# Kernel tuning notes

Hardware: AMD Instinct MI355X
Metric: run time of the kernel (lower is better)

## Reference

```python
import jax, jax.numpy as jnp
import numpy as np

# Contact model constants (from ContactModel defaults / hardcoded values)
STIFFNESS = 100000.0
DISSIPATION = 0.2
STATIC_FRICTION = 0.8
DYNAMIC_FRICTION = 0.8
VISCOUS_FRICTION = 0.5
TRANSITION_VELOCITY = 0.2
GROUND_HEIGHT = 0.0
DT = 0.05
RADIUS = 0.032
EPS = 1e-5
EPS2 = 1e-16
BV = 50.0
BD = 300.0

# 12 spheres: 6 right (bodies 4,5), 6 left (bodies 9,10)
SPHERE_BODY = np.array([4, 4, 4, 4, 5, 5, 9, 9, 9, 9, 10, 10], dtype=np.int32)
SPHERE_LOCAL = np.array([
    [0.00190115788407966, -0.01, -0.00382630379623308],
    [0.148386399942063,   -0.01, -0.028713422052654],
    [0.133001170607051,   -0.01,  0.0516362473449566],
    [0.0662346661991635,  -0.01,  0.0263641606741698],
    [0.06,                -0.01, -0.0187603084619177],
    [0.045,               -0.01,  0.0618569567549652],
    [0.00190115788407966, -0.01,  0.00382630379623308],
    [0.148386399942063,   -0.01,  0.028713422052654],
    [0.133001170607051,   -0.01, -0.0516362473449566],
    [0.0662346661991635,  -0.01, -0.0263641606741698],
    [0.06,                -0.01,  0.0187603084619177],
    [0.045,               -0.01, -0.0618569567549652],
], dtype=np.float32)
NORMAL = np.array([0.0, 1.0, 0.0], dtype=np.float32)


def _sphere_positions(joints, joints_ori):
    # joints: (B,24,3), joints_ori: (B,24,3,3) -> (B,12,3)
    body_pos = joints[:, SPHERE_BODY]            # (B,12,3)
    body_ori = joints_ori[:, SPHERE_BODY]        # (B,12,3,3)
    local = jnp.asarray(SPHERE_LOCAL)
    return body_pos + jnp.einsum('bsij,sj->bsi', body_ori, local)


def _contact_forces(pos, vel):
    # pos, vel: (B,S,3) -> forces (B,S,3); fully vectorized over spheres
    n = jnp.asarray(NORMAL)
    indentation = GROUND_HEIGHT - pos[..., 1]                    # (B,S)
    vnormal = vel[..., 1]                                        # dot(vel, [0,1,0])
    vtangent = vel - vnormal[..., None] * n                      # (B,S,3)
    ind_vel = -vnormal
    k = 0.5 * STIFFNESS ** (2.0 / 3.0)
    # sqrt(ind^2+eps)**1.5 == (ind^2+eps)**0.75
    fH = (4.0 / 3.0) * k * np.sqrt(RADIUS * k) * (indentation * indentation + EPS) ** 0.75
    fHd = fH * (1.0 + 1.5 * DISSIPATION * ind_vel)
    fn = ((0.5 * jnp.tanh(BV * (ind_vel + 1.0 / (1.5 * DISSIPATION))) + 0.5 + EPS2)
          * (0.5 * jnp.tanh(BD * indentation) + 0.5 + EPS2) * fHd)
    vslip = jnp.sqrt(jnp.sum(vtangent * vtangent, axis=-1) + EPS)
    vrel = vslip / TRANSITION_VELOCITY
    ffriction = fn * (jnp.minimum(vrel, 1.0)
                      * (DYNAMIC_FRICTION + 2.0 * (STATIC_FRICTION - DYNAMIC_FRICTION) / (1.0 + vrel * vrel))
                      + VISCOUS_FRICTION * vslip)
    force = fn[..., None] * n
    friction_force = ffriction[..., None] * (-vtangent) / (vslip[..., None] + EPS)
    return force + friction_force


def _cop_and_torque(pos, forces):
    # pos, forces: (B,S,3) -> cop (B,3), torque (B,3); vectorized batch version of the per-b loop
    vf = forces[..., 1]                          # (B,S)
    valid = vf > 0.0
    w = jnp.where(valid, vf, 0.0)
    tw = jnp.sum(w, axis=-1)                     # (B,)
    has = tw > 0.0
    tw_safe = jnp.where(has, tw, 1.0)
    cop_x = jnp.where(has, jnp.sum(pos[..., 0] * w, axis=-1) / tw_safe, 0.0)
    cop_y = jnp.where(has, GROUND_HEIGHT, 0.0)
    cop_z = jnp.where(has, jnp.sum(pos[..., 2] * w, axis=-1) / tw_safe, 0.0)
    cop = jnp.stack([cop_x, cop_y, cop_z], axis=-1)  # (B,3)
    r = pos - cop[:, None, :]
    f_masked = jnp.where(valid[..., None], forces, 0.0)  # only valid contacts contribute torque
    torque = jnp.sum(jnp.cross(r, f_masked), axis=1)
    return cop, torque


def setup_inputs() -> dict:
    key = jax.random.key(0)
    k1, k2 = jax.random.split(key)
    B = 262144
    joints = jax.random.normal(k1, (B, 24, 3), dtype=jnp.float32)
    joints_ori = jax.random.normal(k2, (B, 24, 3, 3), dtype=jnp.float32)
    return {"joints": joints, "joints_ori": joints_ori}


def reference(joints, joints_ori):
    pos = _sphere_positions(joints, joints_ori)              # (B,12,3)
    # finite-difference sphere velocity over frames (dt); zero at first frame
    vel = (pos - jnp.concatenate([pos[:1], pos[:-1]], axis=0)) / DT
    sphere_forces = _contact_forces(pos, vel)                # (B,12,3)

    force = jnp.sum(sphere_forces, axis=1)
    force_right = jnp.sum(sphere_forces[:, :6], axis=1)
    force_left = jnp.sum(sphere_forces[:, 6:], axis=1)
    cop, torque = _cop_and_torque(pos, sphere_forces)
    cop_right, torque_right = _cop_and_torque(pos[:, :6], sphere_forces[:, :6])
    cop_left, torque_left = _cop_and_torque(pos[:, 6:], sphere_forces[:, 6:])
    return (force, torque, cop, sphere_forces, pos,
            force_right, force_left, torque_right, torque_left, cop_right, cop_left)
```

## Files before the change

kernel.cpp:

```cpp
#include <hip/hip_runtime.h>
#include <math.h>


__device__ __constant__ float c_local[12][3] = {
    {0.00190115788407966f, -0.01f, -0.00382630379623308f},
    {0.148386399942063f,   -0.01f, -0.028713422052654f},
    {0.133001170607051f,   -0.01f,  0.0516362473449566f},
    {0.0662346661991635f,  -0.01f,  0.0263641606741698f},
    {0.06f,                -0.01f, -0.0187603084619177f},
    {0.045f,               -0.01f,  0.0618569567549652f},
    {0.00190115788407966f, -0.01f,  0.00382630379623308f},
    {0.148386399942063f,   -0.01f,  0.028713422052654f},
    {0.133001170607051f,   -0.01f, -0.0516362473449566f},
    {0.0662346661991635f,  -0.01f, -0.0263641606741698f},
    {0.06f,                -0.01f,  0.0187603084619177f},
    {0.045f,               -0.01f, -0.0618569567549652f}};

__global__ __launch_bounds__(256)
void contact_kernel(const float* __restrict__ joints,
                    const float* __restrict__ jori,
                    float* __restrict__ out, const int B)
{
    const int b = blockIdx.x * blockDim.x + threadIdx.x;
    if (b >= B) return;

    float px[12], py[12], pz[12];
    float fx[12], fy[12], fz[12];

    {
        const int bodies[4] = {4, 5, 9, 10};
        const int sbeg[4]   = {0, 4, 6, 10};
        const int scnt[4]   = {4, 2, 4, 2};
        const int bp = (b > 0) ? (b - 1) : b;
        const float* jr  = joints + (size_t)b  * 72;
        const float* jrp = joints + (size_t)bp * 72;
        const float* mr  = jori   + (size_t)b  * 216;
        const float* mrp = jori   + (size_t)bp * 216;

        #pragma unroll
        for (int bi = 0; bi < 4; ++bi) {
            const int body = bodies[bi];
            const float jx = jr[body*3+0], jy = jr[body*3+1], jz = jr[body*3+2];
            const float* m = mr + body*9;
            const float m00=m[0],m01=m[1],m02=m[2];
            const float m10=m[3],m11=m[4],m12=m[5];
            const float m20=m[6],m21=m[7],m22=m[8];
            const float kx = jrp[body*3+0], ky = jrp[body*3+1], kz = jrp[body*3+2];
            const float* nn = mrp + body*9;
            const float n00=nn[0],n01=nn[1],n02=nn[2];
            const float n10=nn[3],n11=nn[4],n12=nn[5];
            const float n20=nn[6],n21=nn[7],n22=nn[8];
            #pragma unroll
            for (int si = 0; si < 4; ++si) {
                if (si < scnt[bi]) {
                    const int s = sbeg[bi] + si;
                    const float lx = c_local[s][0];
                    const float ly = c_local[s][1];
                    const float lz = c_local[s][2];
                    const float ax = jx + m00*lx + m01*ly + m02*lz;
                    const float ay = jy + m10*lx + m11*ly + m12*lz;
                    const float az = jz + m20*lx + m21*ly + m22*lz;
                    const float bx = kx + n00*lx + n01*ly + n02*lz;
                    const float by = ky + n10*lx + n11*ly + n12*lz;
                    const float bz = kz + n20*lx + n21*ly + n22*lz;
                    px[s] = ax; py[s] = ay; pz[s] = az;
                    fx[s] = (ax - bx) * 20.0f;
                    fy[s] = (ay - by) * 20.0f;
                    fz[s] = (az - bz) * 20.0f;
                }
            }
        }
    }

    const float KF  = 1077.21734501594f;
    const float CFH = (4.0f/3.0f) * KF * sqrtf(0.032f * KF);
    #pragma unroll
    for (int s = 0; s < 12; ++s) {
        const float vx = fx[s], vy = fy[s], vz = fz[s];
        const float ind     = -py[s];
        const float ind_vel = -vy;
        const float q   = ind*ind + 1e-5f;
        const float fH  = CFH * sqrtf(q * sqrtf(q));
        const float fHd = fH * (1.0f + 0.3f * ind_vel);
        const float t1 = (0.5f*tanhf(50.0f*(ind_vel + 3.3333333333333335f)) + 0.5f) + 1e-16f;
        const float t2 = (0.5f*tanhf(300.0f*ind) + 0.5f) + 1e-16f;
        const float fn = t1 * t2 * fHd;
        const float vslip = sqrtf(vx*vx + vz*vz + 1e-5f);
        const float vrel  = vslip * 5.0f;
        const float mu  = fminf(vrel, 1.0f) * 0.8f + 0.5f * vslip;
        const float ffr = fn * mu;
        const float sc  = ffr / (vslip + 1e-5f);
        fx[s] = -sc * vx;
        fy[s] = fn;
        fz[s] = -sc * vz;
    }

    float res[3][9];
    const int gs0[3] = {0, 0, 6};
    const int gs1[3] = {12, 6, 12};
    #pragma unroll
    for (int g = 0; g < 3; ++g) {
        float Fx=0.f, Fy=0.f, Fz=0.f, tw=0.f, sx=0.f, sz=0.f;
        #pragma unroll
        for (int s = 0; s < 12; ++s) {
            if (s >= gs0[g] && s < gs1[g]) {
                Fx += fx[s]; Fy += fy[s]; Fz += fz[s];
                const float w = fy[s] > 0.f ? fy[s] : 0.f;
                tw += w;
                sx += px[s] * w;
                sz += pz[s] * w;
            }
        }
        const bool has = tw > 0.f;
        const float cx = has ? sx / tw : 0.f;
        const float cz = has ? sz / tw : 0.f;
        float Tx=0.f, Ty=0.f, Tz=0.f;
        #pragma unroll
        for (int s = 0; s < 12; ++s) {
            if (s >= gs0[g] && s < gs1[g]) {
                if (fy[s] > 0.f) {
                    const float rx = px[s]-cx, ry = py[s], rz = pz[s]-cz;
                    Tx += ry*fz[s] - rz*fy[s];
                    Ty += rz*fx[s] - rx*fz[s];
                    Tz += rx*fy[s] - ry*fx[s];
                }
            }
        }
        res[g][0]=Fx; res[g][1]=Fy; res[g][2]=Fz;
        res[g][3]=Tx; res[g][4]=Ty; res[g][5]=Tz;
        res[g][6]=cx; res[g][7]=0.f; res[g][8]=cz;
    }

    const size_t sB = (size_t)B;
    const size_t t3 = (size_t)b * 3;
    float* o;
    o = out;           o[t3]=res[0][0]; o[t3+1]=res[0][1]; o[t3+2]=res[0][2];
    o = out + sB*3;    o[t3]=res[0][3]; o[t3+1]=res[0][4]; o[t3+2]=res[0][5];
    o = out + sB*6;    o[t3]=res[0][6]; o[t3+1]=res[0][7]; o[t3+2]=res[0][8];
    o = out + sB*81;   o[t3]=res[1][0]; o[t3+1]=res[1][1]; o[t3+2]=res[1][2];
    o = out + sB*84;   o[t3]=res[2][0]; o[t3+1]=res[2][1]; o[t3+2]=res[2][2];
    o = out + sB*87;   o[t3]=res[1][3]; o[t3+1]=res[1][4]; o[t3+2]=res[1][5];
    o = out + sB*90;   o[t3]=res[2][3]; o[t3+1]=res[2][4]; o[t3+2]=res[2][5];
    o = out + sB*93;   o[t3]=res[1][6]; o[t3+1]=res[1][7]; o[t3+2]=res[1][8];
    o = out + sB*96;   o[t3]=res[2][6]; o[t3+1]=res[2][7]; o[t3+2]=res[2][8];

    float* osf = out + sB*9  + (size_t)b*36;
    float* opp = out + sB*45 + (size_t)b*36;
    if ((B & 3) == 0) {
        float bufF[36], bufP[36];
        #pragma unroll
        for (int s = 0; s < 12; ++s) {
            bufF[s*3+0]=fx[s]; bufF[s*3+1]=fy[s]; bufF[s*3+2]=fz[s];
            bufP[s*3+0]=px[s]; bufP[s*3+1]=py[s]; bufP[s*3+2]=pz[s];
        }
        #pragma unroll
        for (int i = 0; i < 9; ++i) {
            reinterpret_cast<float4*>(osf)[i] = reinterpret_cast<float4*>(bufF)[i];
            reinterpret_cast<float4*>(opp)[i] = reinterpret_cast<float4*>(bufP)[i];
        }
    } else {
        #pragma unroll
        for (int s = 0; s < 12; ++s) {
            osf[s*3+0]=fx[s]; osf[s*3+1]=fy[s]; osf[s*3+2]=fz[s];
            opp[s*3+0]=px[s]; opp[s*3+1]=py[s]; opp[s*3+2]=pz[s];
        }
    }
}

extern "C" void kernel_launch(void* const* d_in, const int* in_sizes, int n_in,
                              void* d_out, int out_size, void* d_ws, size_t ws_size,
                              hipStream_t stream) {
    const float* joints = (const float*)d_in[0];
    const float* jori   = (const float*)d_in[1];
    float* out = (float*)d_out;
    const int B = in_sizes[0] / 72;
    const int block = 256;
    const int grid  = (B + block - 1) / block;
    contact_kernel<<<grid, block, 0, stream>>>(joints, jori, out, B);
}
```

Baseline: 67.31 us.

## Reuse previous-frame sphere positions via wavefront shuffle instead of reloading

Each 64-lane wavefront now covers 63 consecutive frames plus one halo lane. The previous frame's sphere positions come from __shfl_up across lanes, so the second set of joint and orientation loads and the duplicate transform math are gone. Halo lanes compute but do not write, and frame 0 gets zero velocity because shuffling from lane 0 returns its own value. The constant-memory offset table is replaced by in-register constants. The cost is about 1/64 redundant compute and a new launch-geometry mapping.

```diff
diff --git a/kernel.cpp b/kernel.cpp
--- a/kernel.cpp
+++ b/kernel.cpp
@@ -1,42 +1,36 @@
 #include <hip/hip_runtime.h>
 #include <math.h>
 
-
-__device__ __constant__ float c_local[12][3] = {
-    {0.00190115788407966f, -0.01f, -0.00382630379623308f},
-    {0.148386399942063f,   -0.01f, -0.028713422052654f},
-    {0.133001170607051f,   -0.01f,  0.0516362473449566f},
-    {0.0662346661991635f,  -0.01f,  0.0263641606741698f},
-    {0.06f,                -0.01f, -0.0187603084619177f},
-    {0.045f,               -0.01f,  0.0618569567549652f},
-    {0.00190115788407966f, -0.01f,  0.00382630379623308f},
-    {0.148386399942063f,   -0.01f,  0.028713422052654f},
-    {0.133001170607051f,   -0.01f, -0.0516362473449566f},
-    {0.0662346661991635f,  -0.01f, -0.0263641606741698f},
-    {0.06f,                -0.01f,  0.0187603084619177f},
-    {0.045f,               -0.01f, -0.0618569567549652f}};
 
 __global__ __launch_bounds__(256)
 void contact_kernel(const float* __restrict__ joints,
                     const float* __restrict__ jori,
                     float* __restrict__ out, const int B)
 {
-    const int b = blockIdx.x * blockDim.x + threadIdx.x;
-    if (b >= B) return;
+    const int lane = threadIdx.x & 63;
+    const int wg   = blockIdx.x * 4 + (threadIdx.x >> 6);
+    const long bL  = (long)wg * 63 + lane;
+    const bool do_write = (bL < B) && (lane > 0 || bL == 0);
+    const int  b = (bL < (long)B) ? (int)bL : (B - 1);
 
     float px[12], py[12], pz[12];
     float fx[12], fy[12], fz[12];
 
     {
+        const float c_lx[12] = {0.00190115788407966f, 0.148386399942063f, 0.133001170607051f,
+                                0.0662346661991635f, 0.06f, 0.045f,
+                                0.00190115788407966f, 0.148386399942063f, 0.133001170607051f,
+                                0.0662346661991635f, 0.06f, 0.045f};
+        const float c_lz[12] = {-0.00382630379623308f, -0.028713422052654f, 0.0516362473449566f,
+                                 0.0263641606741698f, -0.0187603084619177f, 0.0618569567549652f,
+                                 0.00382630379623308f, 0.028713422052654f, -0.0516362473449566f,
+                                -0.0263641606741698f, 0.0187603084619177f, -0.0618569567549652f};
+        const float ly = -0.01f;
         const int bodies[4] = {4, 5, 9, 10};
         const int sbeg[4]   = {0, 4, 6, 10};
         const int scnt[4]   = {4, 2, 4, 2};
-        const int bp = (b > 0) ? (b - 1) : b;
-        const float* jr  = joints + (size_t)b  * 72;
-        const float* jrp = joints + (size_t)bp * 72;
-        const float* mr  = jori   + (size_t)b  * 216;
-        const float* mrp = jori   + (size_t)bp * 216;
-
+        const float* jr = joints + (size_t)b * 72;
+        const float* mr = jori   + (size_t)b * 216;
         #pragma unroll
         for (int bi = 0; bi < 4; ++bi) {
             const int body = bodies[bi];
@@ -45,31 +39,24 @@
             const float m00=m[0],m01=m[1],m02=m[2];
             const float m10=m[3],m11=m[4],m12=m[5];
             const float m20=m[6],m21=m[7],m22=m[8];
-            const float kx = jrp[body*3+0], ky = jrp[body*3+1], kz = jrp[body*3+2];
-            const float* nn = mrp + body*9;
-            const float n00=nn[0],n01=nn[1],n02=nn[2];
-            const float n10=nn[3],n11=nn[4],n12=nn[5];
-            const float n20=nn[6],n21=nn[7],n22=nn[8];
             #pragma unroll
             for (int si = 0; si < 4; ++si) {
                 if (si < scnt[bi]) {
                     const int s = sbeg[bi] + si;
-                    const float lx = c_local[s][0];
-                    const float ly = c_local[s][1];
-                    const float lz = c_local[s][2];
-                    const float ax = jx + m00*lx + m01*ly + m02*lz;
-                    const float ay = jy + m10*lx + m11*ly + m12*lz;
-                    const float az = jz + m20*lx + m21*ly + m22*lz;
-                    const float bx = kx + n00*lx + n01*ly + n02*lz;
-                    const float by = ky + n10*lx + n11*ly + n12*lz;
-                    const float bz = kz + n20*lx + n21*ly + n22*lz;
-                    px[s] = ax; py[s] = ay; pz[s] = az;
-                    fx[s] = (ax - bx) * 20.0f;
-                    fy[s] = (ay - by) * 20.0f;
-                    fz[s] = (az - bz) * 20.0f;
+                    const float lx = c_lx[s], lz = c_lz[s];
+                    px[s] = jx + m00*lx + m01*ly + m02*lz;
+                    py[s] = jy + m10*lx + m11*ly + m12*lz;
+                    pz[s] = jz + m20*lx + m21*ly + m22*lz;
                 }
             }
         }
+    }
+
+    #pragma unroll
+    for (int s = 0; s < 12; ++s) {
+        fx[s] = (px[s] - __shfl_up(px[s], 1)) * 20.0f;
+        fy[s] = (py[s] - __shfl_up(py[s], 1)) * 20.0f;
+        fz[s] = (pz[s] - __shfl_up(pz[s], 1)) * 20.0f;
     }
 
     const float KF  = 1077.21734501594f;
@@ -131,38 +118,40 @@
         res[g][6]=cx; res[g][7]=0.f; res[g][8]=cz;
     }
 
-    const size_t sB = (size_t)B;
-    const size_t t3 = (size_t)b * 3;
-    float* o;
-    o = out;           o[t3]=res[0][0]; o[t3+1]=res[0][1]; o[t3+2]=res[0][2];
-    o = out + sB*3;    o[t3]=res[0][3]; o[t3+1]=res[0][4]; o[t3+2]=res[0][5];
-    o = out + sB*6;    o[t3]=res[0][6]; o[t3+1]=res[0][7]; o[t3+2]=res[0][8];
-    o = out + sB*81;   o[t3]=res[1][0]; o[t3+1]=res[1][1]; o[t3+2]=res[1][2];
-    o = out + sB*84;   o[t3]=res[2][0]; o[t3+1]=res[2][1]; o[t3+2]=res[2][2];
-    o = out + sB*87;   o[t3]=res[1][3]; o[t3+1]=res[1][4]; o[t3+2]=res[1][5];
-    o = out + sB*90;   o[t3]=res[2][3]; o[t3+1]=res[2][4]; o[t3+2]=res[2][5];
-    o = out + sB*93;   o[t3]=res[1][6]; o[t3+1]=res[1][7]; o[t3+2]=res[1][8];
-    o = out + sB*96;   o[t3]=res[2][6]; o[t3+1]=res[2][7]; o[t3+2]=res[2][8];
+    if (do_write) {
+        const size_t sB = (size_t)B;
+        const size_t t3 = (size_t)b * 3;
+        float* o;
+        o = out;           o[t3]=res[0][0]; o[t3+1]=res[0][1]; o[t3+2]=res[0][2];
+        o = out + sB*3;    o[t3]=res[0][3]; o[t3+1]=res[0][4]; o[t3+2]=res[0][5];
+        o = out + sB*6;    o[t3]=res[0][6]; o[t3+1]=res[0][7]; o[t3+2]=res[0][8];
+        o = out + sB*81;   o[t3]=res[1][0]; o[t3+1]=res[1][1]; o[t3+2]=res[1][2];
+        o = out + sB*84;   o[t3]=res[2][0]; o[t3+1]=res[2][1]; o[t3+2]=res[2][2];
+        o = out + sB*87;   o[t3]=res[1][3]; o[t3+1]=res[1][4]; o[t3+2]=res[1][5];
+        o = out + sB*90;   o[t3]=res[2][3]; o[t3+1]=res[2][4]; o[t3+2]=res[2][5];
+        o = out + sB*93;   o[t3]=res[1][6]; o[t3+1]=res[1][7]; o[t3+2]=res[1][8];
+        o = out + sB*96;   o[t3]=res[2][6]; o[t3+1]=res[2][7]; o[t3+2]=res[2][8];
 
-    float* osf = out + sB*9  + (size_t)b*36;
-    float* opp = out + sB*45 + (size_t)b*36;
-    if ((B & 3) == 0) {
-        float bufF[36], bufP[36];
-        #pragma unroll
-        for (int s = 0; s < 12; ++s) {
-            bufF[s*3+0]=fx[s]; bufF[s*3+1]=fy[s]; bufF[s*3+2]=fz[s];
-            bufP[s*3+0]=px[s]; bufP[s*3+1]=py[s]; bufP[s*3+2]=pz[s];
-        }
-        #pragma unroll
-        for (int i = 0; i < 9; ++i) {
-            reinterpret_cast<float4*>(osf)[i] = reinterpret_cast<float4*>(bufF)[i];
-            reinterpret_cast<float4*>(opp)[i] = reinterpret_cast<float4*>(bufP)[i];
-        }
-    } else {
-        #pragma unroll
-        for (int s = 0; s < 12; ++s) {
-            osf[s*3+0]=fx[s]; osf[s*3+1]=fy[s]; osf[s*3+2]=fz[s];
-            opp[s*3+0]=px[s]; opp[s*3+1]=py[s]; opp[s*3+2]=pz[s];
+        float* osf = out + sB*9  + (size_t)b*36;
+        float* opp = out + sB*45 + (size_t)b*36;
+        if ((B & 3) == 0) {
+            float bufF[36], bufP[36];
+            #pragma unroll
+            for (int s = 0; s < 12; ++s) {
+                bufF[s*3+0]=fx[s]; bufF[s*3+1]=fy[s]; bufF[s*3+2]=fz[s];
+                bufP[s*3+0]=px[s]; bufP[s*3+1]=py[s]; bufP[s*3+2]=pz[s];
+            }
+            #pragma unroll
+            for (int i = 0; i < 9; ++i) {
+                reinterpret_cast<float4*>(osf)[i] = reinterpret_cast<float4*>(bufF)[i];
+                reinterpret_cast<float4*>(opp)[i] = reinterpret_cast<float4*>(bufP)[i];
+            }
+        } else {
+            #pragma unroll
+            for (int s = 0; s < 12; ++s) {
+                osf[s*3+0]=fx[s]; osf[s*3+1]=fy[s]; osf[s*3+2]=fz[s];
+                opp[s*3+0]=px[s]; opp[s*3+1]=py[s]; opp[s*3+2]=pz[s];
+            }
         }
     }
 }
@@ -174,7 +163,8 @@
     const float* jori   = (const float*)d_in[1];
     float* out = (float*)d_out;
     const int B = in_sizes[0] / 72;
-    const int block = 256;
-    const int grid  = (B + block - 1) / block;
-    contact_kernel<<<grid, block, 0, stream>>>(joints, jori, out, B);
+    long waves = ((long)B + 61) / 63;
+    if (waves < 1) waves = 1;
+    const int blocks = (int)((waves + 3) / 4);
+    contact_kernel<<<blocks, 256, 0, stream>>>(joints, jori, out, B);
 }
```

New measurement: 69.93 us. 3.9% more time.

## Split each frame across two threads, one per foot, combining totals via lane shuffle

Applied to the files above, without the earlier changes.

Each batch frame is now handled by two adjacent threads, one for the right-foot spheres and one for the left. This doubles thread count, cuts per-thread register use and serial work, and improves latency hiding. The whole-body totals are formed by exchanging partial sums with __shfl_xor. The combined torque is rewritten algebraically as the torque about the origin plus a COP correction term, which may change floating-point rounding slightly. Store widths are adjusted so each half writes its 18-float chunk with float4/float2 stores.

```diff
diff --git a/kernel.cpp b/kernel.cpp
--- a/kernel.cpp
+++ b/kernel.cpp
@@ -21,16 +21,19 @@
                     const float* __restrict__ jori,
                     float* __restrict__ out, const int B)
 {
-    const int b = blockIdx.x * blockDim.x + threadIdx.x;
-    if (b >= B) return;
-
-    float px[12], py[12], pz[12];
-    float fx[12], fy[12], fz[12];
+    const long t = (long)blockIdx.x * blockDim.x + threadIdx.x;
+    if (t >= 2L * B) return;
+    const int b = (int)(t >> 1);
+    const int f = (int)(t & 1);
+
+    float px[6], py[6], pz[6];
+    float fx[6], fy[6], fz[6];
 
     {
-        const int bodies[4] = {4, 5, 9, 10};
-        const int sbeg[4]   = {0, 4, 6, 10};
-        const int scnt[4]   = {4, 2, 4, 2};
+        const int body0 = f ? 9 : 4;
+        const int bodies[2] = {body0, body0 + 1};
+        const int sbeg[2]   = {0, 4};
+        const int scnt[2]   = {4, 2};
         const int bp = (b > 0) ? (b - 1) : b;
         const float* jr  = joints + (size_t)b  * 72;
         const float* jrp = joints + (size_t)bp * 72;
@@ -38,7 +41,7 @@
         const float* mrp = jori   + (size_t)bp * 216;
 
         #pragma unroll
-        for (int bi = 0; bi < 4; ++bi) {
+        for (int bi = 0; bi < 2; ++bi) {
             const int body = bodies[bi];
             const float jx = jr[body*3+0], jy = jr[body*3+1], jz = jr[body*3+2];
             const float* m = mr + body*9;
@@ -53,10 +56,11 @@
             #pragma unroll
             for (int si = 0; si < 4; ++si) {
                 if (si < scnt[bi]) {
-                    const int s = sbeg[bi] + si;
-                    const float lx = c_local[s][0];
-                    const float ly = c_local[s][1];
-                    const float lz = c_local[s][2];
+                    const int s  = sbeg[bi] + si;
+                    const int gs = f*6 + s;
+                    const float lx = c_local[gs][0];
+                    const float ly = c_local[gs][1];
+                    const float lz = c_local[gs][2];
                     const float ax = jx + m00*lx + m01*ly + m02*lz;
                     const float ay = jy + m10*lx + m11*ly + m12*lz;
                     const float az = jz + m20*lx + m21*ly + m22*lz;
@@ -75,7 +79,7 @@
     const float KF  = 1077.21734501594f;
     const float CFH = (4.0f/3.0f) * KF * sqrtf(0.032f * KF);
     #pragma unroll
-    for (int s = 0; s < 12; ++s) {
+    for (int s = 0; s < 6; ++s) {
         const float vx = fx[s], vy = fy[s], vz = fz[s];
         const float ind     = -py[s];
         const float ind_vel = -vy;
@@ -95,72 +99,92 @@
         fz[s] = -sc * vz;
     }
 
-    float res[3][9];
-    const int gs0[3] = {0, 0, 6};
-    const int gs1[3] = {12, 6, 12};
+    float SFx=0.f,SFy=0.f,SFz=0.f;
+    float SMx=0.f,SMy=0.f,SMz=0.f;
+    float T0x=0.f,T0y=0.f,T0z=0.f;
+    float tw=0.f, sx=0.f, sz=0.f;
     #pragma unroll
-    for (int g = 0; g < 3; ++g) {
-        float Fx=0.f, Fy=0.f, Fz=0.f, tw=0.f, sx=0.f, sz=0.f;
-        #pragma unroll
-        for (int s = 0; s < 12; ++s) {
-            if (s >= gs0[g] && s < gs1[g]) {
-                Fx += fx[s]; Fy += fy[s]; Fz += fz[s];
-                const float w = fy[s] > 0.f ? fy[s] : 0.f;
-                tw += w;
-                sx += px[s] * w;
-                sz += pz[s] * w;
-            }
-        }
-        const bool has = tw > 0.f;
-        const float cx = has ? sx / tw : 0.f;
-        const float cz = has ? sz / tw : 0.f;
-        float Tx=0.f, Ty=0.f, Tz=0.f;
-        #pragma unroll
-        for (int s = 0; s < 12; ++s) {
-            if (s >= gs0[g] && s < gs1[g]) {
-                if (fy[s] > 0.f) {
-                    const float rx = px[s]-cx, ry = py[s], rz = pz[s]-cz;
-                    Tx += ry*fz[s] - rz*fy[s];
-                    Ty += rz*fx[s] - rx*fz[s];
-                    Tz += rx*fy[s] - ry*fx[s];
-                }
-            }
-        }
-        res[g][0]=Fx; res[g][1]=Fy; res[g][2]=Fz;
-        res[g][3]=Tx; res[g][4]=Ty; res[g][5]=Tz;
-        res[g][6]=cx; res[g][7]=0.f; res[g][8]=cz;
-    }
+    for (int s = 0; s < 6; ++s) {
+        SFx += fx[s]; SFy += fy[s]; SFz += fz[s];
+        if (fy[s] > 0.f) {
+            tw += fy[s]; sx += px[s]*fy[s]; sz += pz[s]*fy[s];
+            SMx += fx[s]; SMy += fy[s]; SMz += fz[s];
+            T0x += py[s]*fz[s] - pz[s]*fy[s];
+            T0y += pz[s]*fx[s] - px[s]*fz[s];
+            T0z += px[s]*fy[s] - py[s]*fx[s];
+        }
+    }
+
+    const bool  hasf = tw > 0.f;
+    const float cxf  = hasf ? sx / tw : 0.f;
+    const float czf  = hasf ? sz / tw : 0.f;
+    float Txf=0.f, Tyf=0.f, Tzf=0.f;
+    #pragma unroll
+    for (int s = 0; s < 6; ++s) {
+        if (fy[s] > 0.f) {
+            const float rx = px[s]-cxf, ry = py[s], rz = pz[s]-czf;
+            Txf += ry*fz[s] - rz*fy[s];
+            Tyf += rz*fx[s] - rx*fz[s];
+            Tzf += rx*fy[s] - ry*fx[s];
+        }
+    }
+
+    const float otw  = __shfl_xor(tw, 1),  osx  = __shfl_xor(sx, 1),  osz  = __shfl_xor(sz, 1);
+    const float oFx  = __shfl_xor(SFx, 1), oFy  = __shfl_xor(SFy, 1), oFz  = __shfl_xor(SFz, 1);
+    const float oMx  = __shfl_xor(SMx, 1), oMy  = __shfl_xor(SMy, 1), oMz  = __shfl_xor(SMz, 1);
+    const float oT0x = __shfl_xor(T0x, 1), oT0y = __shfl_xor(T0y, 1), oT0z = __shfl_xor(T0z, 1);
+    const float twa  = tw + otw;
+    const bool  hasa = twa > 0.f;
+    const float cxa  = hasa ? (sx + osx) / twa : 0.f;
+    const float cza  = hasa ? (sz + osz) / twa : 0.f;
+    const float aMx = SMx + oMx, aMy = SMy + oMy, aMz = SMz + oMz;
+    const float Txa = (T0x + oT0x) + cza*aMy;
+    const float Tya = (T0y + oT0y) - cza*aMx + cxa*aMz;
+    const float Tza = (T0z + oT0z) - cxa*aMy;
 
     const size_t sB = (size_t)B;
     const size_t t3 = (size_t)b * 3;
     float* o;
-    o = out;           o[t3]=res[0][0]; o[t3+1]=res[0][1]; o[t3+2]=res[0][2];
-    o = out + sB*3;    o[t3]=res[0][3]; o[t3+1]=res[0][4]; o[t3+2]=res[0][5];
-    o = out + sB*6;    o[t3]=res[0][6]; o[t3+1]=res[0][7]; o[t3+2]=res[0][8];
-    o = out + sB*81;   o[t3]=res[1][0]; o[t3+1]=res[1][1]; o[t3+2]=res[1][2];
-    o = out + sB*84;   o[t3]=res[2][0]; o[t3+1]=res[2][1]; o[t3+2]=res[2][2];
-    o = out + sB*87;   o[t3]=res[1][3]; o[t3+1]=res[1][4]; o[t3+2]=res[1][5];
-    o = out + sB*90;   o[t3]=res[2][3]; o[t3+1]=res[2][4]; o[t3+2]=res[2][5];
-    o = out + sB*93;   o[t3]=res[1][6]; o[t3+1]=res[1][7]; o[t3+2]=res[1][8];
-    o = out + sB*96;   o[t3]=res[2][6]; o[t3+1]=res[2][7]; o[t3+2]=res[2][8];
-
-    float* osf = out + sB*9  + (size_t)b*36;
-    float* opp = out + sB*45 + (size_t)b*36;
+    o = out + sB*(81 + f*3);  o[t3]=SFx; o[t3+1]=SFy; o[t3+2]=SFz;
+    o = out + sB*(87 + f*3);  o[t3]=Txf; o[t3+1]=Tyf; o[t3+2]=Tzf;
+    o = out + sB*(93 + f*3);  o[t3]=cxf; o[t3+1]=0.f; o[t3+2]=czf;
+    if (f == 0) {
+        o = out;          o[t3]=SFx+oFx; o[t3+1]=SFy+oFy; o[t3+2]=SFz+oFz;
+        o = out + sB*3;   o[t3]=Txa;     o[t3+1]=Tya;     o[t3+2]=Tza;
+        o = out + sB*6;   o[t3]=cxa;     o[t3+1]=0.f;     o[t3+2]=cza;
+    }
+
+    float* osf = out + sB*9  + (size_t)b*36 + f*18;
+    float* opp = out + sB*45 + (size_t)b*36 + f*18;
     if ((B & 3) == 0) {
-        float bufF[36], bufP[36];
+        float bufF[18], bufP[18];
         #pragma unroll
-        for (int s = 0; s < 12; ++s) {
+        for (int s = 0; s < 6; ++s) {
             bufF[s*3+0]=fx[s]; bufF[s*3+1]=fy[s]; bufF[s*3+2]=fz[s];
             bufP[s*3+0]=px[s]; bufP[s*3+1]=py[s]; bufP[s*3+2]=pz[s];
         }
-        #pragma unroll
-        for (int i = 0; i < 9; ++i) {
-            reinterpret_cast<float4*>(osf)[i] = reinterpret_cast<float4*>(bufF)[i];
-            reinterpret_cast<float4*>(opp)[i] = reinterpret_cast<float4*>(bufP)[i];
+        if (f == 0) {
+            #pragma unroll
+            for (int i = 0; i < 4; ++i) {
+                reinterpret_cast<float4*>(osf)[i] = reinterpret_cast<const float4*>(bufF)[i];
+                reinterpret_cast<float4*>(opp)[i] = reinterpret_cast<const float4*>(bufP)[i];
+            }
+            reinterpret_cast<float2*>(osf)[8] = make_float2(bufF[16], bufF[17]);
+            reinterpret_cast<float2*>(opp)[8] = make_float2(bufP[16], bufP[17]);
+        } else {
+            reinterpret_cast<float2*>(osf)[0] = make_float2(bufF[0], bufF[1]);
+            reinterpret_cast<float2*>(opp)[0] = make_float2(bufP[0], bufP[1]);
+            #pragma unroll
+            for (int i = 0; i < 4; ++i) {
+                reinterpret_cast<float4*>(osf + 2)[i] =
+                    make_float4(bufF[2+i*4], bufF[3+i*4], bufF[4+i*4], bufF[5+i*4]);
+                reinterpret_cast<float4*>(opp + 2)[i] =
+                    make_float4(bufP[2+i*4], bufP[3+i*4], bufP[4+i*4], bufP[5+i*4]);
+            }
         }
     } else {
         #pragma unroll
-        for (int s = 0; s < 12; ++s) {
+        for (int s = 0; s < 6; ++s) {
             osf[s*3+0]=fx[s]; osf[s*3+1]=fy[s]; osf[s*3+2]=fz[s];
             opp[s*3+0]=px[s]; opp[s*3+1]=py[s]; opp[s*3+2]=pz[s];
         }
@@ -174,7 +198,8 @@
     const float* jori   = (const float*)d_in[1];
     float* out = (float*)d_out;
     const int B = in_sizes[0] / 72;
-    const int block = 256;
-    const int grid  = (B + block - 1) / block;
+    const long threads = 2L * B;
+    const int  block = 256;
+    const int  grid  = (int)((threads + block - 1) / block);
     contact_kernel<<<grid, block, 0, stream>>>(joints, jori, out, B);
 }
```

Measured after the change: 71.46 us. +6.2%, slower.
